# Optimization experiments

Hardware: AMD Instinct MI355X
Metric: run time of the kernel (lower is better)

The kernel has to match this reference:

```python
import jax, jax.numpy as jnp
import numpy as np

B, D_IN, D_H, D_OUT, D_INT = 1024, 2048, 4096, 2048, 1024


def fwht(x):
    """Fast Walsh-Hadamard transform over a length-2^k vector (unnormalized),
    faithful to the torch chunk/cat butterfly loop."""
    n = x.shape[0]
    k = int(n).bit_length() - 1
    for i in range(k):
        y = x.reshape(2 ** i, 2, -1)        # split butterfly level i
        x = jnp.stack([y[:, 0] + y[:, 1], y[:, 0] - y[:, 1]], axis=1)
    return x.reshape(n)


def fastfood(V, BB, Pi, GG, DD):
    """fastfood_torched: pad -> B*x -> H -> permute -> G* -> H -> slice/scale."""
    LL = BB.shape[0]
    vpad = jnp.zeros((LL,), V.dtype).at[: V.shape[0]].set(V)
    m5 = fwht(fwht(BB * vpad)[Pi] * GG)
    divisor = jnp.sqrt(LL * jnp.sum(GG * GG))
    return m5[:DD] / (divisor * np.sqrt(float(DD) / LL))


def _ff_vars(key, DD):
    LL = 1 << int(np.ceil(np.log2(DD)))
    k1, k2, k3 = jax.random.split(key, 3)
    BB = jnp.where(jax.random.uniform(k1, (LL,)) < 0.5, -1.0, 1.0).astype(jnp.float32)
    Pi = jax.random.permutation(k2, LL).astype(jnp.int32)
    GG = jax.random.normal(k3, (LL,), dtype=jnp.float32)
    return BB, Pi, GG


def setup_inputs():
    key = jax.random.key(0)
    ks = jax.random.split(key, 8)
    x = jax.random.normal(ks[0], (B, D_IN), dtype=jnp.float32)
    V = jax.random.normal(ks[1], (D_INT,), dtype=jnp.float32) * 0.01
    W1_0 = jax.random.normal(ks[2], (D_H, D_IN), dtype=jnp.float32) * 0.02
    b1_0 = jnp.zeros((D_H,), jnp.float32)
    W2_0 = jax.random.normal(ks[3], (D_OUT, D_H), dtype=jnp.float32) * 0.02
    b2_0 = jnp.zeros((D_OUT,), jnp.float32)
    BB_W1, Pi_W1, GG_W1 = _ff_vars(ks[4], D_H * D_IN)
    BB_b1, Pi_b1, GG_b1 = _ff_vars(ks[5], D_H)
    BB_W2, Pi_W2, GG_W2 = _ff_vars(ks[6], D_OUT * D_H)
    BB_b2, Pi_b2, GG_b2 = _ff_vars(ks[7], D_OUT)
    return dict(x=x, V=V, W1_0=W1_0, b1_0=b1_0, W2_0=W2_0, b2_0=b2_0,
                BB_W1=BB_W1, Pi_W1=Pi_W1, GG_W1=GG_W1,
                BB_b1=BB_b1, Pi_b1=Pi_b1, GG_b1=GG_b1,
                BB_W2=BB_W2, Pi_W2=Pi_W2, GG_W2=GG_W2,
                BB_b2=BB_b2, Pi_b2=Pi_b2, GG_b2=GG_b2)


def reference(x, V, W1_0, b1_0, W2_0, b2_0,
              BB_W1, Pi_W1, GG_W1, BB_b1, Pi_b1, GG_b1,
              BB_W2, Pi_W2, GG_W2, BB_b2, Pi_b2, GG_b2):
    # Reconstruct each parameter: theta = theta0 + fastfood(V).view(shape)
    W1 = W1_0 + fastfood(V, BB_W1, Pi_W1, GG_W1, D_H * D_IN).reshape(D_H, D_IN)
    b1 = b1_0 + fastfood(V, BB_b1, Pi_b1, GG_b1, D_H)
    W2 = W2_0 + fastfood(V, BB_W2, Pi_W2, GG_W2, D_OUT * D_H).reshape(D_OUT, D_H)
    b2 = b2_0 + fastfood(V, BB_b2, Pi_b2, GG_b2, D_OUT)
    # Wrapped module forward (2-layer MLP)
    h = jax.nn.relu(x @ W1.T + b1)
    return h @ W2.T + b2
```

## Files before the change

kernel.cpp:

```cpp
#include <hip/hip_runtime.h>
#include <hip/hip_bf16.h>
#include <stdint.h>


typedef __attribute__((ext_vector_type(8))) short bf16x8;
typedef __attribute__((ext_vector_type(8))) short short8;
typedef __attribute__((ext_vector_type(4))) float f32x4;

__device__ __forceinline__ ushort f2bf(float f) {
  union { float f; uint32_t u; } v; v.f = f;
  return (ushort)((v.u + 0x7FFFu + ((v.u >> 16) & 1u)) >> 16);
}
__device__ __forceinline__ float bf2f(ushort u) {
  union { uint32_t u; float f; } v; v.u = (uint32_t)u << 16; return v.f;
}

__device__ __forceinline__ void gload_lds16(const void* g, void* l) {
  __builtin_amdgcn_global_load_lds(
      (const __attribute__((address_space(1))) void*)g,
      (__attribute__((address_space(3))) void*)l, 16, 0, 0);
}

__device__ __forceinline__ void wait_vm16() { asm volatile("s_waitcnt vmcnt(16)" ::: "memory"); }
__device__ __forceinline__ void wait_vm8()  { asm volatile("s_waitcnt vmcnt(8)"  ::: "memory"); }
__device__ __forceinline__ void wait_vm0()  { asm volatile("s_waitcnt vmcnt(0)"  ::: "memory"); }
__device__ __forceinline__ void wait_lgkm0(){ asm volatile("s_waitcnt lgkmcnt(0)" ::: "memory"); }
__device__ __forceinline__ void barrier_raw(){ asm volatile("s_barrier" ::: "memory"); }

template <int NN>
__device__ __forceinline__ void wht_inreg(float* v) {
#pragma unroll
  for (int h = 1; h < NN; h <<= 1)
#pragma unroll
    for (int g = 0; g < NN; g += (h << 1))
#pragma unroll
      for (int k = 0; k < h; ++k) {
        float a = v[g + k], b = v[g + k + h];
        v[g + k] = a + b; v[g + k + h] = a - b;
      }
}

__global__ __launch_bounds__(256) void make_t_kernel(
    const float* __restrict__ V, const float* __restrict__ BB1,
    const float* __restrict__ BB2, float* __restrict__ t1, float* __restrict__ t2) {
  __shared__ float ts[1024];
  const float* BB = blockIdx.x ? BB2 : BB1;
  float* t = blockIdx.x ? t2 : t1;
  int tid = threadIdx.x;
  for (int i = tid; i < 1024; i += 256) ts[i] = BB[i] * V[i];
  for (int st = 0; st < 10; ++st) {
    int half = 1 << st;
    __syncthreads();
    for (int j = tid; j < 512; j += 256) {
      int p = ((j >> st) << (st + 1)) | (j & (half - 1));
      float a = ts[p], b = ts[p + half];
      ts[p] = a + b; ts[p + half] = a - b;
    }
  }
  __syncthreads();
  for (int i = tid; i < 1024; i += 256) t[i] = ts[i];
}

__global__ __launch_bounds__(256) void make_bias_kernel(
    const float* __restrict__ V,
    const float* __restrict__ BB1, const int* __restrict__ Pi1, const float* __restrict__ GG1, const float* __restrict__ b10,
    const float* __restrict__ BB2, const int* __restrict__ Pi2, const float* __restrict__ GG2, const float* __restrict__ b20,
    float* __restrict__ ob1, float* __restrict__ ob2) {
  __shared__ float ts[1024];
  __shared__ float zs[4096];
  __shared__ float red[4];
  int tid = threadIdx.x;
  int which = blockIdx.x;
  int L = which ? 2048 : 4096;
  const float* BB = which ? BB2 : BB1;
  const int* Pi = which ? Pi2 : Pi1;
  const float* GG = which ? GG2 : GG1;
  const float* b0 = which ? b20 : b10;
  float* ob = which ? ob2 : ob1;

  for (int i = tid; i < 1024; i += 256) ts[i] = BB[i] * V[i];
  for (int st = 0; st < 10; ++st) {
    int half = 1 << st;
    __syncthreads();
    for (int j = tid; j < 512; j += 256) {
      int p = ((j >> st) << (st + 1)) | (j & (half - 1));
      float a = ts[p], b = ts[p + half];
      ts[p] = a + b; ts[p + half] = a - b;
    }
  }
  __syncthreads();
  float gsum = 0.f;
  for (int i = tid; i < L; i += 256) {
    int pi = Pi[i];
    float g = GG[i];
    gsum += g * g;
    zs[i] = ts[pi & 1023] * g;
  }
  for (int o = 32; o > 0; o >>= 1) gsum += __shfl_down(gsum, o);
  if ((tid & 63) == 0) red[tid >> 6] = gsum;
  __syncthreads();
  float ssum = red[0] + red[1] + red[2] + red[3];
  for (int st = 0; (1 << st) < L; ++st) {
    int half = 1 << st;
    __syncthreads();
    for (int j = tid; j < (L >> 1); j += 256) {
      int p = ((j >> st) << (st + 1)) | (j & (half - 1));
      float a = zs[p], b = zs[p + half];
      zs[p] = a + b; zs[p + half] = a - b;
    }
  }
  __syncthreads();
  float scale = rsqrtf((float)L * ssum);
  for (int i = tid; i < L; i += 256) ob[i] = b0[i] + zs[i] * scale;
}

__device__ __forceinline__ void p1_load(const int* __restrict__ Pi,
                                        const float* __restrict__ GG,
                                        size_t base, int s, int4* p4, float4* g4) {
  const int4* Pi4 = (const int4*)(Pi + base);
  const float4* GG4 = (const float4*)(GG + base);
#pragma unroll
  for (int j = 0; j < 8; ++j) { p4[j] = Pi4[(s << 3) + j]; g4[j] = GG4[(s << 3) + j]; }
}

__device__ __forceinline__ void p1_process(
    float* ts, float* zs, float* red, int tid, bool barA,
    const int4* p4, const float4* g4, ushort* __restrict__ inter, size_t base,
    float* __restrict__ partials, int chunkIdx) {
  float v[32];
  float gsum = 0.f;
#pragma unroll
  for (int j = 0; j < 8; ++j) {
    gsum += g4[j].x * g4[j].x + g4[j].y * g4[j].y + g4[j].z * g4[j].z + g4[j].w * g4[j].w;
    v[4 * j + 0] = ts[p4[j].x & 1023] * g4[j].x;
    v[4 * j + 1] = ts[p4[j].y & 1023] * g4[j].y;
    v[4 * j + 2] = ts[p4[j].z & 1023] * g4[j].z;
    v[4 * j + 3] = ts[p4[j].w & 1023] * g4[j].w;
  }
  wht_inreg<32>(v);
  for (int o = 32; o > 0; o >>= 1) gsum += __shfl_down(gsum, o);

  if (barA) __syncthreads();
  if ((tid & 63) == 0) red[tid >> 6] = gsum;
#pragma unroll
  for (int j = 0; j < 16; ++j) {
    float2 u; u.x = v[2 * j]; u.y = v[2 * j + 1];
    *(float2*)&zs[34 * tid + 2 * j] = u;
  }
  __syncthreads();
  if (tid == 0) partials[chunkIdx] = red[0] + red[1] + red[2] + red[3];

  {
    const int pb = (tid & 31) + 1088 * (tid >> 5);
#pragma unroll
    for (int r = 0; r < 32; ++r) v[r] = zs[pb + 34 * r];
    wht_inreg<32>(v);
#pragma unroll
    for (int r = 0; r < 32; ++r) zs[pb + 34 * r] = v[r];
  }
  __syncthreads();

  {
    const int pc = 4 * tid + 2 * (tid >> 3);
    float w[4][8];
#pragma unroll
    for (int r = 0; r < 8; ++r) {
      float2 u0 = *(const float2*)&zs[pc + 1088 * r];
      float2 u1 = *(const float2*)&zs[pc + 1088 * r + 2];
      w[0][r] = u0.x; w[1][r] = u0.y; w[2][r] = u1.x; w[3][r] = u1.y;
    }
#pragma unroll
    for (int k = 0; k < 4; ++k) wht_inreg<8>(w[k]);
    ushort* op = inter + base + 4 * tid;
#pragma unroll
    for (int r = 0; r < 8; ++r) {
      short4 o;
      o.x = (short)f2bf(w[0][r]); o.y = (short)f2bf(w[1][r]);
      o.z = (short)f2bf(w[2][r]); o.w = (short)f2bf(w[3][r]);
      *(short4*)&op[r << 10] = o;
    }
  }
}

__global__ __launch_bounds__(256) void ff_pass1(
    const int* __restrict__ Pi1, const float* __restrict__ GG1,
    const int* __restrict__ Pi2, const float* __restrict__ GG2,
    const float* __restrict__ t1, const float* __restrict__ t2,
    ushort* __restrict__ inter1, ushort* __restrict__ inter2,
    float* __restrict__ partials) {
  __shared__ float ts[1024];
  __shared__ float zs[8704];
  __shared__ float red[4];
  const int tid = threadIdx.x;
  const int wsel = blockIdx.x >> 9;
  const int b = blockIdx.x & 511;
  const int* Pi = wsel ? Pi2 : Pi1;
  const float* GG = wsel ? GG2 : GG1;
  const float* t = wsel ? t2 : t1;
  ushort* inter = wsel ? inter2 : inter1;
  const size_t base0 = (size_t)(b * 2) << 13;
  const size_t base1 = (size_t)(b * 2 + 1) << 13;
  const int ci = (wsel << 10) + b * 2;

  for (int i = tid; i < 1024; i += 256) ts[i] = t[i];
  int4 pa[8]; float4 ga[8];
  p1_load(Pi, GG, base0, tid, pa, ga);
  __syncthreads();
  int4 pb[8]; float4 gb[8];
  p1_load(Pi, GG, base1, tid, pb, gb);
  p1_process(ts, zs, red, tid, false, pa, ga, inter, base0, partials, ci);
  p1_process(ts, zs, red, tid, true,  pb, gb, inter, base1, partials, ci + 1);
}

__global__ __launch_bounds__(512) void ff_pass2(
    const ushort* __restrict__ inter1, const ushort* __restrict__ inter2,
    const float* __restrict__ W01, const float* __restrict__ W02,
    const float* __restrict__ partials,
    ushort* __restrict__ W1b, ushort* __restrict__ W2b) {
  __shared__ ushort tile[1024][34];
  __shared__ float red[8];
  const int tid = threadIdx.x;
  const int wsel = blockIdx.x >> 8;
  const int cb = (blockIdx.x & 255) << 5;
  const ushort* inter = wsel ? inter2 : inter1;
  const float* W0 = wsel ? W02 : W01;
  ushort* Wb = wsel ? W2b : W1b;

  float s = partials[(wsel << 10) + tid] + partials[(wsel << 10) + tid + 512];
  for (int o = 32; o > 0; o >>= 1) s += __shfl_down(s, o);
  if ((tid & 63) == 0) red[tid >> 6] = s;

  const int p = tid & 15;
  const int g = tid >> 4;
  const ushort* ip = inter + ((size_t)(g << 5) << 13) + cb + (p << 1);
  float va[32], vb[32];
#pragma unroll
  for (int r = 0; r < 32; ++r) {
    ushort2 u = *(const ushort2*)(ip + ((size_t)r << 13));
    va[r] = bf2f(u.x); vb[r] = bf2f(u.y);
  }
  wht_inreg<32>(va);
  wht_inreg<32>(vb);
#pragma unroll
  for (int r = 0; r < 32; ++r) {
    ushort2 u; u.x = f2bf(va[r]); u.y = f2bf(vb[r]);
    *(ushort2*)&tile[(g << 5) + r][p << 1] = u;
  }
  __syncthreads();
  float ssum = 0.f;
#pragma unroll
  for (int k = 0; k < 8; ++k) ssum += red[k];
  const float sc = rsqrtf(8388608.f * ssum);

  float wa[32], wb[32];
#pragma unroll
  for (int r = 0; r < 32; ++r) {
    ushort2 u = *(const ushort2*)&tile[g + (r << 5)][p << 1];
    wa[r] = bf2f(u.x); wb[r] = bf2f(u.y);
  }
  wht_inreg<32>(wa);
  wht_inreg<32>(wb);
#pragma unroll
  for (int r = 0; r < 32; ++r) {
    size_t m = (((size_t)(g + (r << 5))) << 13) + cb + (p << 1);
    float2 w0 = *(const float2*)(W0 + m);
    ushort2 u;
    u.x = f2bf(wa[r] * sc + w0.x);
    u.y = f2bf(wb[r] * sc + w0.y);
    *(ushort2*)(Wb + m) = u;
  }
}

__global__ __launch_bounds__(256) void cvt_f32_bf16(
    const float4* __restrict__ in, ushort4* __restrict__ out, int n4) {
  int i = blockIdx.x * 256 + threadIdx.x;
  if (i < n4) {
    float4 v = in[i];
    ushort4 o;
    o.x = f2bf(v.x); o.y = f2bf(v.y); o.z = f2bf(v.z); o.w = f2bf(v.w);
    out[i] = o;
  }
}

template <int EPI, int NT>
__global__ __launch_bounds__(256) void gemm_bt(
    const ushort* __restrict__ A, const ushort* __restrict__ B,
    const float* __restrict__ bias, ushort* __restrict__ Cb, float* __restrict__ Cf,
    int M, int N, int K) {
  __shared__ ushort As[4][8192];
  __shared__ ushort Bs[4][8192];
  const int tid = threadIdx.x;
  const int w = tid >> 6, l = tid & 63;
  const int wr = w >> 1, wc = w & 1;
  const int brow = blockIdx.y << 7, bcol = blockIdx.x << 7;
  const int lrow = l >> 3;
  const int csrc = ((l & 7) ^ lrow) << 3;
  const int l15 = l & 15;
  const int x7 = l15 & 7;
  const int kb = blockIdx.z * (NT << 6);
  f32x4 acc[4][4] = {};

  const ushort* pa = A + (size_t)(brow + (w << 5) + lrow) * K + kb + csrc;
  const ushort* pb = B + (size_t)(bcol + (w << 5) + lrow) * K + kb + csrc;
  const size_t K8 = (size_t)K << 3;

#define STAGE(buf, tt)                                                      \
  {                                                                         \
    const ushort* qa = pa + ((tt) << 6);                                    \
    const ushort* qb = pb + ((tt) << 6);                                    \
    _Pragma("unroll")                                                       \
    for (int i = 0; i < 4; ++i) {                                           \
      gload_lds16(qa + K8 * i, &As[buf][(((w << 2) + i) << 9)]);            \
      gload_lds16(qb + K8 * i, &Bs[buf][(((w << 2) + i) << 9)]);            \
    }                                                                       \
  }

  STAGE(0, 0); STAGE(1, 1); STAGE(2, 2);
  for (int t = 0; t < NT; ++t) {
    if (t < NT - 2) wait_vm16();
    else if (t == NT - 2) wait_vm8();
    else wait_vm0();
    barrier_raw();
    if (t + 3 < NT) STAGE((t + 3) & 3, t + 3);
    const ushort* Acur = As[t & 3];
    const ushort* Bcur = Bs[t & 3];
    bf16x8 af[2][4], bfr[2][4];
#pragma unroll
    for (int kk = 0; kk < 2; ++kk) {
      int c8 = (kk << 2) + (l >> 4);
#pragma unroll
      for (int m = 0; m < 4; ++m)
        af[kk][m] = *(const bf16x8*)&Acur[(((wr << 6) + (m << 4) + l15) << 6) + ((c8 ^ x7) << 3)];
#pragma unroll
      for (int n = 0; n < 4; ++n)
        bfr[kk][n] = *(const bf16x8*)&Bcur[(((wc << 6) + (n << 4) + l15) << 6) + ((c8 ^ x7) << 3)];
    }
    wait_lgkm0();
#pragma unroll
    for (int kk = 0; kk < 2; ++kk)
#pragma unroll
      for (int m = 0; m < 4; ++m)
#pragma unroll
        for (int n = 0; n < 4; ++n)
          acc[m][n] = __builtin_amdgcn_mfma_f32_16x16x32_bf16(af[kk][m], bfr[kk][n], acc[m][n], 0, 0, 0);
  }
#undef STAGE

  if (EPI == 0) {
#pragma unroll
    for (int n = 0; n < 4; ++n) {
      int col = bcol + (wc << 6) + (n << 4) + l15;
      float bv = bias[col];
#pragma unroll
      for (int m = 0; m < 4; ++m) {
        int row0 = brow + (wr << 6) + (m << 4) + ((l >> 4) << 2);
#pragma unroll
        for (int j = 0; j < 4; ++j) {
          float vv = fmaxf(acc[m][n][j] + bv, 0.f);
          Cb[(size_t)(row0 + j) * N + col] = f2bf(vv);
        }
      }
    }
  } else {
    float* outp = Cf + (size_t)blockIdx.z * M * N;
#pragma unroll
    for (int n = 0; n < 4; ++n) {
      int col = bcol + (wc << 6) + (n << 4) + l15;
#pragma unroll
      for (int m = 0; m < 4; ++m) {
        int row0 = brow + (wr << 6) + (m << 4) + ((l >> 4) << 2);
#pragma unroll
        for (int j = 0; j < 4; ++j)
          outp[(size_t)(row0 + j) * N + col] = acc[m][n][j];
      }
    }
  }
}

__global__ __launch_bounds__(256) void reduce_out(
    const float4* __restrict__ P, const float* __restrict__ b2,
    float4* __restrict__ out) {
  int i = blockIdx.x * 256 + threadIdx.x;
  float4 a = P[i], b = P[i + 524288];
  const float4 bb = *(const float4*)(b2 + ((i & 511) << 2));
  float4 o;
  o.x = a.x + b.x + bb.x; o.y = a.y + b.y + bb.y;
  o.z = a.z + b.z + bb.z; o.w = a.w + b.w + bb.w;
  out[i] = o;
}

extern "C" void kernel_launch(void* const* d_in, const int* in_sizes, int n_in,
                              void* d_out, int out_size, void* d_ws, size_t ws_size,
                              hipStream_t stream) {
  const float* x     = (const float*)d_in[0];
  const float* V     = (const float*)d_in[1];
  const float* W1_0  = (const float*)d_in[2];
  const float* b1_0  = (const float*)d_in[3];
  const float* W2_0  = (const float*)d_in[4];
  const float* b2_0  = (const float*)d_in[5];
  const float* BB_W1 = (const float*)d_in[6];
  const int*   Pi_W1 = (const int*)d_in[7];
  const float* GG_W1 = (const float*)d_in[8];
  const float* BB_b1 = (const float*)d_in[9];
  const int*   Pi_b1 = (const int*)d_in[10];
  const float* GG_b1 = (const float*)d_in[11];
  const float* BB_W2 = (const float*)d_in[12];
  const int*   Pi_W2 = (const int*)d_in[13];
  const float* GG_W2 = (const float*)d_in[14];
  const float* BB_b2 = (const float*)d_in[15];
  const int*   Pi_b2 = (const int*)d_in[16];
  const float* GG_b2 = (const float*)d_in[17];
  float* out = (float*)d_out;

  const size_t MB = 1048576ull;
  char* ws = (char*)d_ws;
  ushort* inter1 = (ushort*)(ws);
  float*  P      = (float*)(ws);
  ushort* inter2 = (ushort*)(ws + 16 * MB);
  ushort* W1b    = (ushort*)(ws + 32 * MB);
  ushort* W2b    = (ushort*)(ws + 48 * MB);
  ushort* xb     = (ushort*)(ws + 64 * MB);
  ushort* hb     = (ushort*)(ws + 68 * MB);
  char*   S      = ws + 76 * MB;
  float*  t1     = (float*)(S);
  float*  t2     = (float*)(S + 4096);
  float*  b1     = (float*)(S + 8192);
  float*  b2     = (float*)(S + 8192 + 16384);
  float*  parts  = (float*)(S + 8192 + 16384 + 8192);

  make_t_kernel<<<2, 256, 0, stream>>>(V, BB_W1, BB_W2, t1, t2);
  make_bias_kernel<<<2, 256, 0, stream>>>(V, BB_b1, Pi_b1, GG_b1, b1_0,
                                          BB_b2, Pi_b2, GG_b2, b2_0, b1, b2);
  cvt_f32_bf16<<<2048, 256, 0, stream>>>((const float4*)x, (ushort4*)xb, 524288);

  ff_pass1<<<1024, 256, 0, stream>>>(Pi_W1, GG_W1, Pi_W2, GG_W2, t1, t2,
                                     inter1, inter2, parts);
  ff_pass2<<<512, 512, 0, stream>>>(inter1, inter2, W1_0, W2_0, parts, W1b, W2b);

  gemm_bt<0, 32><<<dim3(32, 8, 1), 256, 0, stream>>>(xb, W1b, b1, hb, nullptr, 1024, 4096, 2048);
  gemm_bt<1, 32><<<dim3(16, 8, 2), 256, 0, stream>>>(hb, W2b, nullptr, nullptr, P, 1024, 2048, 4096);
  reduce_out<<<2048, 256, 0, stream>>>((const float4*)P, b2, (float4*)out);
}
```

Baseline: 174.2 us.

## Merge prep kernels and software-pipeline fastfood pass1 over four chunks per block

Fuses the t-vector, bias and x-to-bf16 conversion kernels into one launch, removing two launch gaps. ff_pass1 now handles four 8192-element chunks per block (512 blocks instead of 1024) and prefetches the Pi/GG loads for the next chunk while the current one goes through the LDS butterfly stages. __syncthreads is replaced by an explicit lgkmcnt wait plus s_barrier with a sched_barrier, so outstanding global prefetches are not drained at each barrier. The cost is higher register pressure from two in-flight chunk buffers and half as many blocks, which means less parallelism.

```diff
diff --git a/kernel.cpp b/kernel.cpp
--- a/kernel.cpp
+++ b/kernel.cpp
@@ -4,7 +4,6 @@
 
 
 typedef __attribute__((ext_vector_type(8))) short bf16x8;
-typedef __attribute__((ext_vector_type(8))) short short8;
 typedef __attribute__((ext_vector_type(4))) float f32x4;
 
 __device__ __forceinline__ ushort f2bf(float f) {
@@ -26,6 +25,11 @@
 __device__ __forceinline__ void wait_vm0()  { asm volatile("s_waitcnt vmcnt(0)"  ::: "memory"); }
 __device__ __forceinline__ void wait_lgkm0(){ asm volatile("s_waitcnt lgkmcnt(0)" ::: "memory"); }
 __device__ __forceinline__ void barrier_raw(){ asm volatile("s_barrier" ::: "memory"); }
+__device__ __forceinline__ void lds_barrier() {
+  wait_lgkm0();
+  barrier_raw();
+  __builtin_amdgcn_sched_barrier(0);
+}
 
 template <int NN>
 __device__ __forceinline__ void wht_inreg(float* v) {
@@ -40,78 +44,94 @@
       }
 }
 
-__global__ __launch_bounds__(256) void make_t_kernel(
-    const float* __restrict__ V, const float* __restrict__ BB1,
-    const float* __restrict__ BB2, float* __restrict__ t1, float* __restrict__ t2) {
-  __shared__ float ts[1024];
-  const float* BB = blockIdx.x ? BB2 : BB1;
-  float* t = blockIdx.x ? t2 : t1;
-  int tid = threadIdx.x;
-  for (int i = tid; i < 1024; i += 256) ts[i] = BB[i] * V[i];
-  for (int st = 0; st < 10; ++st) {
-    int half = 1 << st;
-    __syncthreads();
-    for (int j = tid; j < 512; j += 256) {
-      int p = ((j >> st) << (st + 1)) | (j & (half - 1));
-      float a = ts[p], b = ts[p + half];
-      ts[p] = a + b; ts[p + half] = a - b;
-    }
-  }
-  __syncthreads();
-  for (int i = tid; i < 1024; i += 256) t[i] = ts[i];
-}
-
-__global__ __launch_bounds__(256) void make_bias_kernel(
+__global__ __launch_bounds__(256) void prep(
+    const float4* __restrict__ x4, ushort4* __restrict__ xb4,
     const float* __restrict__ V,
-    const float* __restrict__ BB1, const int* __restrict__ Pi1, const float* __restrict__ GG1, const float* __restrict__ b10,
-    const float* __restrict__ BB2, const int* __restrict__ Pi2, const float* __restrict__ GG2, const float* __restrict__ b20,
+    const float* __restrict__ BBW1, const float* __restrict__ BBW2,
+    float* __restrict__ t1, float* __restrict__ t2,
+    const float* __restrict__ BBb1, const int* __restrict__ Pib1,
+    const float* __restrict__ GGb1, const float* __restrict__ b10,
+    const float* __restrict__ BBb2, const int* __restrict__ Pib2,
+    const float* __restrict__ GGb2, const float* __restrict__ b20,
     float* __restrict__ ob1, float* __restrict__ ob2) {
   __shared__ float ts[1024];
   __shared__ float zs[4096];
   __shared__ float red[4];
-  int tid = threadIdx.x;
-  int which = blockIdx.x;
-  int L = which ? 2048 : 4096;
-  const float* BB = which ? BB2 : BB1;
-  const int* Pi = which ? Pi2 : Pi1;
-  const float* GG = which ? GG2 : GG1;
-  const float* b0 = which ? b20 : b10;
-  float* ob = which ? ob2 : ob1;
-
-  for (int i = tid; i < 1024; i += 256) ts[i] = BB[i] * V[i];
-  for (int st = 0; st < 10; ++st) {
-    int half = 1 << st;
+  const int bid = blockIdx.x;
+  const int tid = threadIdx.x;
+
+  if (bid < 2048) {
+    int i = bid * 256 + tid;
+    float4 v = x4[i];
+    ushort4 o;
+    o.x = f2bf(v.x); o.y = f2bf(v.y); o.z = f2bf(v.z); o.w = f2bf(v.w);
+    xb4[i] = o;
+    return;
+  }
+
+  if (bid < 2050) {
+    const int which = bid - 2048;
+    const float* BB = which ? BBW2 : BBW1;
+    float* t = which ? t2 : t1;
+    for (int i = tid; i < 1024; i += 256) ts[i] = BB[i] * V[i];
+    for (int st = 0; st < 10; ++st) {
+      int half = 1 << st;
+      __syncthreads();
+      for (int j = tid; j < 512; j += 256) {
+        int p = ((j >> st) << (st + 1)) | (j & (half - 1));
+        float a = ts[p], b = ts[p + half];
+        ts[p] = a + b; ts[p + half] = a - b;
+      }
+    }
     __syncthreads();
-    for (int j = tid; j < 512; j += 256) {
-      int p = ((j >> st) << (st + 1)) | (j & (half - 1));
-      float a = ts[p], b = ts[p + half];
-      ts[p] = a + b; ts[p + half] = a - b;
-    }
-  }
-  __syncthreads();
-  float gsum = 0.f;
-  for (int i = tid; i < L; i += 256) {
-    int pi = Pi[i];
-    float g = GG[i];
-    gsum += g * g;
-    zs[i] = ts[pi & 1023] * g;
-  }
-  for (int o = 32; o > 0; o >>= 1) gsum += __shfl_down(gsum, o);
-  if ((tid & 63) == 0) red[tid >> 6] = gsum;
-  __syncthreads();
-  float ssum = red[0] + red[1] + red[2] + red[3];
-  for (int st = 0; (1 << st) < L; ++st) {
-    int half = 1 << st;
+    for (int i = tid; i < 1024; i += 256) t[i] = ts[i];
+    return;
+  }
+
+  {
+    const int which = bid - 2050;
+    const int L = which ? 2048 : 4096;
+    const float* BB = which ? BBb2 : BBb1;
+    const int* Pi = which ? Pib2 : Pib1;
+    const float* GG = which ? GGb2 : GGb1;
+    const float* b0 = which ? b20 : b10;
+    float* ob = which ? ob2 : ob1;
+
+    for (int i = tid; i < 1024; i += 256) ts[i] = BB[i] * V[i];
+    for (int st = 0; st < 10; ++st) {
+      int half = 1 << st;
+      __syncthreads();
+      for (int j = tid; j < 512; j += 256) {
+        int p = ((j >> st) << (st + 1)) | (j & (half - 1));
+        float a = ts[p], b = ts[p + half];
+        ts[p] = a + b; ts[p + half] = a - b;
+      }
+    }
     __syncthreads();
-    for (int j = tid; j < (L >> 1); j += 256) {
-      int p = ((j >> st) << (st + 1)) | (j & (half - 1));
-      float a = zs[p], b = zs[p + half];
-      zs[p] = a + b; zs[p + half] = a - b;
-    }
-  }
-  __syncthreads();
-  float scale = rsqrtf((float)L * ssum);
-  for (int i = tid; i < L; i += 256) ob[i] = b0[i] + zs[i] * scale;
+    float gsum = 0.f;
+    for (int i = tid; i < L; i += 256) {
+      int pi = Pi[i];
+      float g = GG[i];
+      gsum += g * g;
+      zs[i] = ts[pi & 1023] * g;
+    }
+    for (int o = 32; o > 0; o >>= 1) gsum += __shfl_down(gsum, o);
+    if ((tid & 63) == 0) red[tid >> 6] = gsum;
+    __syncthreads();
+    float ssum = red[0] + red[1] + red[2] + red[3];
+    for (int st = 0; (1 << st) < L; ++st) {
+      int half = 1 << st;
+      __syncthreads();
+      for (int j = tid; j < (L >> 1); j += 256) {
+        int p = ((j >> st) << (st + 1)) | (j & (half - 1));
+        float a = zs[p], b = zs[p + half];
+        zs[p] = a + b; zs[p + half] = a - b;
+      }
+    }
+    __syncthreads();
+    float scale = rsqrtf((float)L * ssum);
+    for (int i = tid; i < L; i += 256) ob[i] = b0[i] + zs[i] * scale;
+  }
 }
 
 __device__ __forceinline__ void p1_load(const int* __restrict__ Pi,
@@ -123,11 +143,8 @@
   for (int j = 0; j < 8; ++j) { p4[j] = Pi4[(s << 3) + j]; g4[j] = GG4[(s << 3) + j]; }
 }
 
-__device__ __forceinline__ void p1_process(
-    float* ts, float* zs, float* red, int tid, bool barA,
-    const int4* p4, const float4* g4, ushort* __restrict__ inter, size_t base,
-    float* __restrict__ partials, int chunkIdx) {
-  float v[32];
+__device__ __forceinline__ float p1_gather(const float* ts, const int4* p4,
+                                           const float4* g4, float* v) {
   float gsum = 0.f;
 #pragma unroll
   for (int j = 0; j < 8; ++j) {
@@ -139,15 +156,21 @@
   }
   wht_inreg<32>(v);
   for (int o = 32; o > 0; o >>= 1) gsum += __shfl_down(gsum, o);
-
-  if (barA) __syncthreads();
-  if ((tid & 63) == 0) red[tid >> 6] = gsum;
+  return gsum;
+}
+
+__device__ __forceinline__ void p1_lds(
+    float* zs, float* red, int tid, float* v, float gs,
+    ushort* __restrict__ inter, size_t base,
+    float* __restrict__ partials, int chunkIdx) {
+  lds_barrier();
+  if ((tid & 63) == 0) red[tid >> 6] = gs;
 #pragma unroll
   for (int j = 0; j < 16; ++j) {
     float2 u; u.x = v[2 * j]; u.y = v[2 * j + 1];
     *(float2*)&zs[34 * tid + 2 * j] = u;
   }
-  __syncthreads();
+  lds_barrier();
   if (tid == 0) partials[chunkIdx] = red[0] + red[1] + red[2] + red[3];
 
   {
@@ -158,7 +181,7 @@
 #pragma unroll
     for (int r = 0; r < 32; ++r) zs[pb + 34 * r] = v[r];
   }
-  __syncthreads();
+  lds_barrier();
 
   {
     const int pc = 4 * tid + 2 * (tid >> 3);
@@ -192,24 +215,33 @@
   __shared__ float zs[8704];
   __shared__ float red[4];
   const int tid = threadIdx.x;
-  const int wsel = blockIdx.x >> 9;
-  const int b = blockIdx.x & 511;
+  const int wsel = blockIdx.x >> 8;
+  const int b = blockIdx.x & 255;
   const int* Pi = wsel ? Pi2 : Pi1;
   const float* GG = wsel ? GG2 : GG1;
   const float* t = wsel ? t2 : t1;
   ushort* inter = wsel ? inter2 : inter1;
-  const size_t base0 = (size_t)(b * 2) << 13;
-  const size_t base1 = (size_t)(b * 2 + 1) << 13;
-  const int ci = (wsel << 10) + b * 2;
-
+  const int c0 = b << 2;
+  const int pbase = (wsel << 10) + c0;
+
+  int4 pA[8]; float4 gA[8]; int4 pB[8]; float4 gB[8];
   for (int i = tid; i < 1024; i += 256) ts[i] = t[i];
-  int4 pa[8]; float4 ga[8];
-  p1_load(Pi, GG, base0, tid, pa, ga);
+  p1_load(Pi, GG, (size_t)(c0 + 0) << 13, tid, pA, gA);
+  p1_load(Pi, GG, (size_t)(c0 + 1) << 13, tid, pB, gB);
   __syncthreads();
-  int4 pb[8]; float4 gb[8];
-  p1_load(Pi, GG, base1, tid, pb, gb);
-  p1_process(ts, zs, red, tid, false, pa, ga, inter, base0, partials, ci);
-  p1_process(ts, zs, red, tid, true,  pb, gb, inter, base1, partials, ci + 1);
+
+  float v[32];
+  float gs;
+  gs = p1_gather(ts, pA, gA, v);
+  p1_load(Pi, GG, (size_t)(c0 + 2) << 13, tid, pA, gA);
+  p1_lds(zs, red, tid, v, gs, inter, (size_t)(c0 + 0) << 13, partials, pbase + 0);
+  gs = p1_gather(ts, pB, gB, v);
+  p1_load(Pi, GG, (size_t)(c0 + 3) << 13, tid, pB, gB);
+  p1_lds(zs, red, tid, v, gs, inter, (size_t)(c0 + 1) << 13, partials, pbase + 1);
+  gs = p1_gather(ts, pA, gA, v);
+  p1_lds(zs, red, tid, v, gs, inter, (size_t)(c0 + 2) << 13, partials, pbase + 2);
+  gs = p1_gather(ts, pB, gB, v);
+  p1_lds(zs, red, tid, v, gs, inter, (size_t)(c0 + 3) << 13, partials, pbase + 3);
 }
 
 __global__ __launch_bounds__(512) void ff_pass2(
@@ -268,17 +300,6 @@
     u.x = f2bf(wa[r] * sc + w0.x);
     u.y = f2bf(wb[r] * sc + w0.y);
     *(ushort2*)(Wb + m) = u;
-  }
-}
-
-__global__ __launch_bounds__(256) void cvt_f32_bf16(
-    const float4* __restrict__ in, ushort4* __restrict__ out, int n4) {
-  int i = blockIdx.x * 256 + threadIdx.x;
-  if (i < n4) {
-    float4 v = in[i];
-    ushort4 o;
-    o.x = f2bf(v.x); o.y = f2bf(v.y); o.z = f2bf(v.z); o.w = f2bf(v.w);
-    out[i] = o;
   }
 }
 
@@ -428,13 +449,13 @@
   float*  b2     = (float*)(S + 8192 + 16384);
   float*  parts  = (float*)(S + 8192 + 16384 + 8192);
 
-  make_t_kernel<<<2, 256, 0, stream>>>(V, BB_W1, BB_W2, t1, t2);
-  make_bias_kernel<<<2, 256, 0, stream>>>(V, BB_b1, Pi_b1, GG_b1, b1_0,
-                                          BB_b2, Pi_b2, GG_b2, b2_0, b1, b2);
-  cvt_f32_bf16<<<2048, 256, 0, stream>>>((const float4*)x, (ushort4*)xb, 524288);
-
-  ff_pass1<<<1024, 256, 0, stream>>>(Pi_W1, GG_W1, Pi_W2, GG_W2, t1, t2,
-                                     inter1, inter2, parts);
+  prep<<<2052, 256, 0, stream>>>((const float4*)x, (ushort4*)xb, V,
+                                 BB_W1, BB_W2, t1, t2,
+                                 BB_b1, Pi_b1, GG_b1, b1_0,
+                                 BB_b2, Pi_b2, GG_b2, b2_0, b1, b2);
+
+  ff_pass1<<<512, 256, 0, stream>>>(Pi_W1, GG_W1, Pi_W2, GG_W2, t1, t2,
+                                    inter1, inter2, parts);
   ff_pass2<<<512, 512, 0, stream>>>(inter1, inter2, W1_0, W2_0, parts, W1b, W2b);
 
   gemm_bt<0, 32><<<dim3(32, 8, 1), 256, 0, stream>>>(xb, W1b, b1, hb, nullptr, 1024, 4096, 2048);
```

Result: no change. 172.9 us (-0.8%).
